# Kernel optimization log

Hardware: AMD Instinct MI355X
Metric: run time of the kernel (lower is better)

## Reference

```python
import jax, jax.numpy as jnp
import numpy as np

B, S, D, H, K = 16, 2048, 1024, 16, 31  # batch, seq, d_model, n_heads, kernel_size


def setup_inputs() -> dict:
    key = jax.random.key(0)
    ks = jax.random.split(key, 6)
    sc = 1.0 / np.sqrt(D)
    return {
        "query_sequences": jax.random.normal(ks[0], (B, S, D), jnp.float32),
        "key_sequences": jax.random.normal(ks[1], (B, S, D), jnp.float32),
        "value_sequences": jax.random.normal(ks[2], (B, S, D), jnp.float32),
        "key_value_sequence_lengths": jax.random.randint(ks[3], (B,), 1, S + 1, jnp.int32),
        "W_q": jax.random.normal(ks[4], (D, H * K), jnp.float32) * sc,  # cast_queries.weight^T
        "b_q": jnp.zeros((H * K,), jnp.float32),                        # cast_queries.bias
        "conv_bias": jnp.zeros((H,), jnp.float32),
    }


def reference(query_sequences, key_sequences, value_sequences,
              key_value_sequence_lengths, W_q, b_q, conv_bias):
    b, s, d = query_sequences.shape
    h = conv_bias.shape[0]
    k = W_q.shape[1] // h
    r = d // h
    # Generate per-position, per-head depthwise filters from the queries.
    weights = (query_sequences @ W_q + b_q).reshape(b, s, h, k)  # (B,S,H,K)
    # Split key channels into heads and reduce within each head -> (B,S,H)
    ksum = key_sequences.reshape(b, s, h, r).sum(axis=-1)
    pad_l = (k - 1) // 2
    pad_r = k - 1 - pad_l
    kpad = jnp.pad(ksum, ((0, 0), (pad_l, pad_r), (0, 0)))  # (B, S+K-1, H)
    # Cross-correlation with per-position filters:
    # out[b,t,h] = sum_j weights[b,t,h,j] * kpad[b, t+j, h]
    out = jnp.zeros((b, s, h), dtype=weights.dtype)
    for j in range(k):  # fixed small kernel loop
        out = out + weights[..., j] * kpad[:, j:j + s, :]
    out = out + conv_bias  # per-head bias
    return out.transpose(0, 2, 1)  # (B, n_heads, S)
```

## Files before the change

### kernel.cpp

```cpp
#include <hip/hip_runtime.h>
#include <hip/hip_bf16.h>

#define BB 16
#define SS 2048
#define DD 1024
#define HH 16
#define KK 31
#define HK 496

typedef float f32x16 __attribute__((ext_vector_type(16)));
typedef __bf16 bf16x8 __attribute__((ext_vector_type(8)));

__device__ __forceinline__ unsigned f2bf(float x) {
  unsigned u = __float_as_uint(x);
  unsigned r = u + 0x7FFFu + ((u >> 16) & 1u);
  return r >> 16;
}

__global__ void prep_kernel(const float* __restrict__ Wq,
                            unsigned short* __restrict__ Bimg) {
  int idx = blockIdx.x * 256 + threadIdx.x;
  int e = idx & 7;
  int lane = (idx >> 3) & 63;
  int nt = (idx >> 9) & 1;
  int w = (idx >> 10) & 7;
  int slice = (idx >> 13) & 1;
  int ks = idx >> 14;
  int k = ks * 32 + slice * 16 + (lane >> 5) * 8 + e;
  int c = w * 64 + nt * 32 + (lane & 31);
  int h = c >> 5, j = c & 31;
  float v = (j < KK) ? Wq[k * HK + h * KK + j] : 0.f;
  Bimg[idx] = (unsigned short)f2bf(v);
}

__global__ void ksum_kernel(const float* __restrict__ key,
                            float* __restrict__ ksum) {
  const int row = blockIdx.x;
  const int tid = threadIdx.x;
  const float4 v = reinterpret_cast<const float4*>(key + (size_t)row * DD)[tid];
  float p = v.x + v.y + v.z + v.w;
  p += __shfl_xor(p, 1);
  p += __shfl_xor(p, 2);
  p += __shfl_xor(p, 4);
  p += __shfl_xor(p, 8);
  if ((tid & 15) == 0) ksum[(size_t)row * HH + (tid >> 4)] = p;
}

__global__ __launch_bounds__(512, 4) void mca_kernel(
    const float* __restrict__ q, const float* __restrict__ bq,
    const float* __restrict__ convb, const float* __restrict__ ksum,
    const unsigned short* __restrict__ Bimg, float* __restrict__ out) {
  __shared__ char smem[8192];
  const int tid = threadIdx.x;
  const int w = tid >> 6, lane = tid & 63;
  const int l31 = lane & 31, hi = lane >> 5;
  const int bid = blockIdx.x;
  const int bb = bid >> 5;
  const int t0 = (bid & 31) << 6;

  char* const bA0 = smem;
  char* const bA1 = smem + 4096;

  const float* qblk = q + ((size_t)(bb * SS + t0)) * DD;
  const unsigned short* bbase = Bimg + (((size_t)w * 2) << 9) + lane * 8;

  f32x16 acc[2][2];
#pragma unroll
  for (int mt = 0; mt < 2; ++mt)
#pragma unroll
    for (int nt = 0; nt < 2; ++nt)
#pragma unroll
      for (int r = 0; r < 16; ++r) acc[mt][nt][r] = 0.f;

  const int arow = tid >> 3;
  const int ak4 = tid & 7;
  const int as = ak4 >> 2, ah = (ak4 >> 1) & 1, ae = ak4 & 1;
  const int abyte = as * 2048 + ah * 1024 + arow * 16 + ae * 8;

  auto issueA = [&](int ks, float4& rA) {
    rA = *reinterpret_cast<const float4*>(qblk + (size_t)arow * DD + ks * 32 + ak4 * 4);
  };
  auto writeA = [&](char* dst, const float4& rA) {
    unsigned u0 = f2bf(rA.x) | (f2bf(rA.y) << 16);
    unsigned u1 = f2bf(rA.z) | (f2bf(rA.w) << 16);
    *reinterpret_cast<uint2*>(dst + abyte) = make_uint2(u0, u1);
  };
  auto loadB = [&](int ks, bf16x8 pB[2][2]) {
    const unsigned short* p = bbase + (size_t)ks * 16384;
#pragma unroll
    for (int s = 0; s < 2; ++s)
#pragma unroll
      for (int nt = 0; nt < 2; ++nt)
        pB[s][nt] = *reinterpret_cast<const bf16x8*>(p + (s * 16 + nt) * 512);
  };
  auto computeT = [&](const char* bufA, const bf16x8 pB[2][2]) {
#pragma unroll
    for (int s = 0; s < 2; ++s) {
      bf16x8 a[2];
#pragma unroll
      for (int mt = 0; mt < 2; ++mt)
        a[mt] = *reinterpret_cast<const bf16x8*>(
            bufA + s * 2048 + hi * 1024 + (mt * 32 + l31) * 16);
#pragma unroll
      for (int mt = 0; mt < 2; ++mt)
#pragma unroll
        for (int nt = 0; nt < 2; ++nt)
          acc[mt][nt] = __builtin_amdgcn_mfma_f32_32x32x16_bf16(
              a[mt], pB[s][nt], acc[mt][nt], 0, 0, 0);
    }
  };
  auto barrier = [&]() {
    asm volatile("s_waitcnt lgkmcnt(0)" ::: "memory");
    __builtin_amdgcn_s_barrier();
  };

  float4 rA0, rA1;
  bf16x8 pBa[2][2], pBb[2][2];

  issueA(0, rA0);
  loadB(0, pBa);
  writeA(bA0, rA0);
  barrier();

  for (int ks2 = 0; ks2 < 15; ++ks2) {
    const int ks = ks2 * 2;
    issueA(ks + 1, rA1);
    loadB(ks + 1, pBb);
    computeT(bA0, pBa);
    writeA(bA1, rA1);
    barrier();
    issueA(ks + 2, rA0);
    loadB(ks + 2, pBa);
    computeT(bA1, pBb);
    writeA(bA0, rA0);
    barrier();
  }
  issueA(31, rA1);
  loadB(31, pBb);
  computeT(bA0, pBa);
  writeA(bA1, rA1);
  barrier();
  computeT(bA1, pBb);

  float bqv[2], cb[2];
#pragma unroll
  for (int nt = 0; nt < 2; ++nt) {
    const int h = w * 2 + nt;
    bqv[nt] = (l31 < KK) ? bq[h * KK + l31] : 0.f;
    cb[nt] = convb[h];
  }

  __syncthreads();
  float* kl = reinterpret_cast<float*>(smem);
  for (int i = tid; i < 96 * 16; i += 512) {
    int trow = i >> 4, h = i & 15;
    int t = t0 + trow - 15;
    kl[trow * 17 + h] = (t >= 0 && t < SS) ? ksum[((size_t)bb * SS + t) * HH + h] : 0.f;
  }
  __syncthreads();

#pragma unroll
  for (int mt = 0; mt < 2; ++mt)
#pragma unroll
    for (int nt = 0; nt < 2; ++nt) {
      const int h = w * 2 + nt;
#pragma unroll
      for (int r = 0; r < 16; ++r) {
        const int tl = mt * 32 + (r & 3) + 8 * (r >> 2) + 4 * hi;
        float v = (acc[mt][nt][r] + bqv[nt]) * kl[(tl + l31) * 17 + h];
        v += __shfl_xor(v, 1);
        v += __shfl_xor(v, 2);
        v += __shfl_xor(v, 4);
        v += __shfl_xor(v, 8);
        v += __shfl_xor(v, 16);
        if (l31 == r)
          out[((size_t)(bb * HH + h)) * SS + t0 + tl] = v + cb[nt];
      }
    }
}

extern "C" void kernel_launch(void* const* d_in, const int* in_sizes, int n_in,
                              void* d_out, int out_size, void* d_ws, size_t ws_size,
                              hipStream_t stream) {
  const float* q   = (const float*)d_in[0];
  const float* key = (const float*)d_in[1];
  const float* Wq  = (const float*)d_in[4];
  const float* bq  = (const float*)d_in[5];
  const float* cvb = (const float*)d_in[6];
  float* out = (float*)d_out;

  float* ksum = (float*)d_ws;
  unsigned short* Bimg = (unsigned short*)((char*)d_ws + (2 << 20));

  prep_kernel<<<2048, 256, 0, stream>>>(Wq, Bimg);
  ksum_kernel<<<BB * SS, 256, 0, stream>>>(key, ksum);
  mca_kernel<<<BB * (SS / 64), 512, 0, stream>>>(q, bq, cvb, ksum, Bimg, out);
}
```

Measured before the change: 90.31 us.

## Split heads across two blocks with 256-wide K stages and swizzled LDS

Splits the 16 heads between two blocks per 64-row tile, so each wave computes one head, and doubles the grid. The A tile is now staged 256 K-columns at a time in 32 KB double buffers with an XOR swizzle, so there are far fewer barriers. B fragments are prefetched four steps ahead in a ring of registers. Nontemporal loads and stores are added for the key reads and output writes. In exchange, each Q tile is read twice from global memory (once per head half), and each block needs 64 KB of dynamic LDS, which reduces occupancy.

```diff
diff --git a/kernel.cpp b/kernel.cpp
--- a/kernel.cpp
+++ b/kernel.cpp
@@ -9,6 +9,7 @@
 #define HK 496
 
 typedef float f32x16 __attribute__((ext_vector_type(16)));
+typedef float f32x4 __attribute__((ext_vector_type(4)));
 typedef __bf16 bf16x8 __attribute__((ext_vector_type(8)));
 
 __device__ __forceinline__ unsigned f2bf(float x) {
@@ -22,13 +23,13 @@
   int idx = blockIdx.x * 256 + threadIdx.x;
   int e = idx & 7;
   int lane = (idx >> 3) & 63;
-  int nt = (idx >> 9) & 1;
-  int w = (idx >> 10) & 7;
-  int slice = (idx >> 13) & 1;
-  int ks = idx >> 14;
-  int k = ks * 32 + slice * 16 + (lane >> 5) * 8 + e;
-  int c = w * 64 + nt * 32 + (lane & 31);
-  int h = c >> 5, j = c & 31;
+  int h8 = (idx >> 9) & 7;
+  int s = (idx >> 12) & 1;
+  int ks = (idx >> 13) & 31;
+  int nb = (idx >> 18) & 1;
+  int k = ks * 32 + s * 16 + (lane >> 5) * 8 + e;
+  int h = nb * 8 + h8;
+  int j = lane & 31;
   float v = (j < KK) ? Wq[k * HK + h * KK + j] : 0.f;
   Bimg[idx] = (unsigned short)f2bf(v);
 }
@@ -37,7 +38,8 @@
                             float* __restrict__ ksum) {
   const int row = blockIdx.x;
   const int tid = threadIdx.x;
-  const float4 v = reinterpret_cast<const float4*>(key + (size_t)row * DD)[tid];
+  const f32x4 v = __builtin_nontemporal_load(
+      reinterpret_cast<const f32x4*>(key + (size_t)row * DD) + tid);
   float p = v.x + v.y + v.z + v.w;
   p += __shfl_xor(p, 1);
   p += __shfl_xor(p, 2);
@@ -50,132 +52,138 @@
     const float* __restrict__ q, const float* __restrict__ bq,
     const float* __restrict__ convb, const float* __restrict__ ksum,
     const unsigned short* __restrict__ Bimg, float* __restrict__ out) {
-  __shared__ char smem[8192];
+  extern __shared__ char smem[];
   const int tid = threadIdx.x;
   const int w = tid >> 6, lane = tid & 63;
   const int l31 = lane & 31, hi = lane >> 5;
   const int bid = blockIdx.x;
-  const int bb = bid >> 5;
-  const int t0 = (bid & 31) << 6;
-
-  char* const bA0 = smem;
-  char* const bA1 = smem + 4096;
+  const int nb = bid & 1;
+  const int mb = bid >> 1;
+  const int bb = mb >> 5;
+  const int t0 = (mb & 31) << 6;
+
+  char* const buf0 = smem;
+  char* const buf1 = smem + 32768;
 
   const float* qblk = q + ((size_t)(bb * SS + t0)) * DD;
-  const unsigned short* bbase = Bimg + (((size_t)w * 2) << 9) + lane * 8;
-
-  f32x16 acc[2][2];
+  const unsigned short* bbase = Bimg + (size_t)nb * 262144 + w * 512 + lane * 8;
+
+  f32x16 acc[2];
 #pragma unroll
   for (int mt = 0; mt < 2; ++mt)
 #pragma unroll
-    for (int nt = 0; nt < 2; ++nt)
-#pragma unroll
-      for (int r = 0; r < 16; ++r) acc[mt][nt][r] = 0.f;
-
-  const int arow = tid >> 3;
-  const int ak4 = tid & 7;
-  const int as = ak4 >> 2, ah = (ak4 >> 1) & 1, ae = ak4 & 1;
-  const int abyte = as * 2048 + ah * 1024 + arow * 16 + ae * 8;
-
-  auto issueA = [&](int ks, float4& rA) {
-    rA = *reinterpret_cast<const float4*>(qblk + (size_t)arow * DD + ks * 32 + ak4 * 4);
-  };
-  auto writeA = [&](char* dst, const float4& rA) {
-    unsigned u0 = f2bf(rA.x) | (f2bf(rA.y) << 16);
-    unsigned u1 = f2bf(rA.z) | (f2bf(rA.w) << 16);
-    *reinterpret_cast<uint2*>(dst + abyte) = make_uint2(u0, u1);
-  };
-  auto loadB = [&](int ks, bf16x8 pB[2][2]) {
-    const unsigned short* p = bbase + (size_t)ks * 16384;
+    for (int r = 0; r < 16; ++r) acc[mt][r] = 0.f;
+
+  f32x4 rq[4];
+
+  auto issueA = [&](int p, int hf) {
+#pragma unroll
+    for (int it = 0; it < 4; ++it) {
+      const int gidx = hf * 2048 + it * 512 + tid;
+      const int row = gidx >> 6, c16 = gidx & 63;
+      rq[it] = *reinterpret_cast<const f32x4*>(qblk + (size_t)row * DD + p * 256 + c16 * 4);
+    }
+  };
+  auto writeA = [&](char* dst, int hf) {
+#pragma unroll
+    for (int it = 0; it < 4; ++it) {
+      const int gidx = hf * 2048 + it * 512 + tid;
+      const int row = gidx >> 6, c16 = gidx & 63;
+      const int ksl = c16 >> 3, sl = (c16 >> 2) & 1, h2 = (c16 >> 1) & 1, e2 = c16 & 1;
+      int byte = ksl * 4096 + sl * 2048 + h2 * 1024 + row * 16 + e2 * 8;
+      byte ^= (h2 << 4) ^ (sl << 5) ^ ((ksl & 1) << 6) ^ (((ksl >> 1) & 1) << 7) ^
+              (((ksl >> 2) & 1) << 8);
+      unsigned u0 = f2bf(rq[it].x) | (f2bf(rq[it].y) << 16);
+      unsigned u1 = f2bf(rq[it].z) | (f2bf(rq[it].w) << 16);
+      *reinterpret_cast<uint2*>(dst + byte) = make_uint2(u0, u1);
+    }
+  };
+
+  bf16x8 Bs[4][2];
+  auto loadB = [&](int ks, int slot) {
 #pragma unroll
     for (int s = 0; s < 2; ++s)
-#pragma unroll
-      for (int nt = 0; nt < 2; ++nt)
-        pB[s][nt] = *reinterpret_cast<const bf16x8*>(p + (s * 16 + nt) * 512);
-  };
-  auto computeT = [&](const char* bufA, const bf16x8 pB[2][2]) {
-#pragma unroll
-    for (int s = 0; s < 2; ++s) {
-      bf16x8 a[2];
-#pragma unroll
-      for (int mt = 0; mt < 2; ++mt)
-        a[mt] = *reinterpret_cast<const bf16x8*>(
-            bufA + s * 2048 + hi * 1024 + (mt * 32 + l31) * 16);
-#pragma unroll
-      for (int mt = 0; mt < 2; ++mt)
-#pragma unroll
-        for (int nt = 0; nt < 2; ++nt)
-          acc[mt][nt] = __builtin_amdgcn_mfma_f32_32x32x16_bf16(
-              a[mt], pB[s][nt], acc[mt][nt], 0, 0, 0);
-    }
-  };
-  auto barrier = [&]() {
+      Bs[slot][s] = *reinterpret_cast<const bf16x8*>(bbase + (size_t)ks * 8192 + s * 4096);
+  };
+  auto dsA = [&](const char* buf, int ksl, int s, int mt) -> bf16x8 {
+    int byte = ksl * 4096 + s * 2048 + hi * 1024 + (mt * 32 + l31) * 16;
+    byte ^= (hi << 4) ^ (s << 5) ^ ((ksl & 1) << 6) ^ (((ksl >> 1) & 1) << 7) ^
+            (((ksl >> 2) & 1) << 8);
+    return *reinterpret_cast<const bf16x8*>(buf + byte);
+  };
+  auto lbar = [&]() {
     asm volatile("s_waitcnt lgkmcnt(0)" ::: "memory");
     __builtin_amdgcn_s_barrier();
-  };
-
-  float4 rA0, rA1;
-  bf16x8 pBa[2][2], pBb[2][2];
-
-  issueA(0, rA0);
-  loadB(0, pBa);
-  writeA(bA0, rA0);
-  barrier();
-
-  for (int ks2 = 0; ks2 < 15; ++ks2) {
-    const int ks = ks2 * 2;
-    issueA(ks + 1, rA1);
-    loadB(ks + 1, pBb);
-    computeT(bA0, pBa);
-    writeA(bA1, rA1);
-    barrier();
-    issueA(ks + 2, rA0);
-    loadB(ks + 2, pBa);
-    computeT(bA1, pBb);
-    writeA(bA0, rA0);
-    barrier();
+    asm volatile("" ::: "memory");
+  };
+
+  loadB(0, 0);
+  loadB(1, 1);
+  loadB(2, 2);
+  loadB(3, 3);
+  issueA(0, 0);
+  writeA(buf0, 0);
+  issueA(0, 1);
+  writeA(buf0, 1);
+  lbar();
+
+#pragma unroll
+  for (int p = 0; p < 4; ++p) {
+    char* cur = (p & 1) ? buf1 : buf0;
+    char* nxt = (p & 1) ? buf0 : buf1;
+    if (p < 3) issueA(p + 1, 0);
+#pragma unroll
+    for (int st = 0; st < 8; ++st) {
+      const int ks = p * 8 + st;
+      const int slot = ks & 3;
+      bf16x8 a00 = dsA(cur, st, 0, 0);
+      bf16x8 a10 = dsA(cur, st, 0, 1);
+      acc[0] = __builtin_amdgcn_mfma_f32_32x32x16_bf16(a00, Bs[slot][0], acc[0], 0, 0, 0);
+      acc[1] = __builtin_amdgcn_mfma_f32_32x32x16_bf16(a10, Bs[slot][0], acc[1], 0, 0, 0);
+      bf16x8 a01 = dsA(cur, st, 1, 0);
+      bf16x8 a11 = dsA(cur, st, 1, 1);
+      acc[0] = __builtin_amdgcn_mfma_f32_32x32x16_bf16(a01, Bs[slot][1], acc[0], 0, 0, 0);
+      acc[1] = __builtin_amdgcn_mfma_f32_32x32x16_bf16(a11, Bs[slot][1], acc[1], 0, 0, 0);
+      if (ks + 4 < 32) loadB(ks + 4, slot);
+      if (st == 3 && p < 3) {
+        writeA(nxt, 0);
+        issueA(p + 1, 1);
+      }
+    }
+    if (p < 3) {
+      writeA(nxt, 1);
+      lbar();
+    }
   }
-  issueA(31, rA1);
-  loadB(31, pBb);
-  computeT(bA0, pBa);
-  writeA(bA1, rA1);
-  barrier();
-  computeT(bA1, pBb);
-
-  float bqv[2], cb[2];
-#pragma unroll
-  for (int nt = 0; nt < 2; ++nt) {
-    const int h = w * 2 + nt;
-    bqv[nt] = (l31 < KK) ? bq[h * KK + l31] : 0.f;
-    cb[nt] = convb[h];
-  }
+
+  const int h = nb * 8 + w;
+  const float bqv = (l31 < KK) ? bq[h * KK + l31] : 0.f;
+  const float cbv = convb[h];
 
   __syncthreads();
   float* kl = reinterpret_cast<float*>(smem);
-  for (int i = tid; i < 96 * 16; i += 512) {
-    int trow = i >> 4, h = i & 15;
+  for (int i = tid; i < 96 * 8; i += 512) {
+    int trow = i >> 3, h8 = i & 7;
     int t = t0 + trow - 15;
-    kl[trow * 17 + h] = (t >= 0 && t < SS) ? ksum[((size_t)bb * SS + t) * HH + h] : 0.f;
+    kl[trow * 9 + h8] =
+        (t >= 0 && t < SS) ? ksum[((size_t)bb * SS + t) * HH + nb * 8 + h8] : 0.f;
   }
   __syncthreads();
 
 #pragma unroll
   for (int mt = 0; mt < 2; ++mt)
 #pragma unroll
-    for (int nt = 0; nt < 2; ++nt) {
-      const int h = w * 2 + nt;
-#pragma unroll
-      for (int r = 0; r < 16; ++r) {
-        const int tl = mt * 32 + (r & 3) + 8 * (r >> 2) + 4 * hi;
-        float v = (acc[mt][nt][r] + bqv[nt]) * kl[(tl + l31) * 17 + h];
-        v += __shfl_xor(v, 1);
-        v += __shfl_xor(v, 2);
-        v += __shfl_xor(v, 4);
-        v += __shfl_xor(v, 8);
-        v += __shfl_xor(v, 16);
-        if (l31 == r)
-          out[((size_t)(bb * HH + h)) * SS + t0 + tl] = v + cb[nt];
-      }
+    for (int r = 0; r < 16; ++r) {
+      const int tl = mt * 32 + (r & 3) + 8 * (r >> 2) + 4 * hi;
+      float v = (acc[mt][r] + bqv) * kl[(tl + l31) * 9 + w];
+      v += __shfl_xor(v, 1);
+      v += __shfl_xor(v, 2);
+      v += __shfl_xor(v, 4);
+      v += __shfl_xor(v, 8);
+      v += __shfl_xor(v, 16);
+      if (l31 == r)
+        __builtin_nontemporal_store(v + cbv,
+                                    out + ((size_t)(bb * HH + h)) * SS + t0 + tl);
     }
 }
 
@@ -192,7 +200,10 @@
   float* ksum = (float*)d_ws;
   unsigned short* Bimg = (unsigned short*)((char*)d_ws + (2 << 20));
 
+  hipFuncSetAttribute((const void*)mca_kernel,
+                      hipFuncAttributeMaxDynamicSharedMemorySize, 65536);
+
   prep_kernel<<<2048, 256, 0, stream>>>(Wq, Bimg);
   ksum_kernel<<<BB * SS, 256, 0, stream>>>(key, ksum);
-  mca_kernel<<<BB * (SS / 64), 512, 0, stream>>>(q, bq, cvb, ksum, Bimg, out);
-}
+  mca_kernel<<<BB * (SS / 64) * 2, 512, 65536, stream>>>(q, bq, cvb, ksum, Bimg, out);
+}
```

New measurement: 123.1 us. 36.3% more time.

## Stage A and B tiles via direct global-to-LDS loads with double buffering

Applied to the files above, without the earlier changes.

Replaces register-staged loads of Q (fp32→bf16 converted before LDS writes) and per-thread B fragment loads with global_load_lds async copies into double-buffered LDS. Q is kept fp32 in LDS with an XOR swizzle and converted to bf16 at fragment read time, and vmcnt waits pipeline the next stage behind compute. The ksum kernel is also changed to process 16 rows per block. This raises LDS use to 80KB per block, which lowers occupancy, and adds conversion work on every fragment read.

```diff
diff --git a/kernel.cpp b/kernel.cpp
--- a/kernel.cpp
+++ b/kernel.cpp
@@ -9,12 +9,19 @@
 #define HK 496
 
 typedef float f32x16 __attribute__((ext_vector_type(16)));
+typedef float f32x4 __attribute__((ext_vector_type(4)));
 typedef __bf16 bf16x8 __attribute__((ext_vector_type(8)));
 
 __device__ __forceinline__ unsigned f2bf(float x) {
   unsigned u = __float_as_uint(x);
   unsigned r = u + 0x7FFFu + ((u >> 16) & 1u);
   return r >> 16;
+}
+
+__device__ __forceinline__ void gll16(const void* g, void* l) {
+  __builtin_amdgcn_global_load_lds(
+      (const __attribute__((address_space(1))) unsigned int*)g,
+      (__attribute__((address_space(3))) unsigned int*)l, 16, 0, 0);
 }
 
 __global__ void prep_kernel(const float* __restrict__ Wq,
@@ -33,24 +40,28 @@
   Bimg[idx] = (unsigned short)f2bf(v);
 }
 
-__global__ void ksum_kernel(const float* __restrict__ key,
-                            float* __restrict__ ksum) {
-  const int row = blockIdx.x;
+__global__ __launch_bounds__(256) void ksum_kernel(const float* __restrict__ key,
+                                                   float* __restrict__ ksum) {
   const int tid = threadIdx.x;
-  const float4 v = reinterpret_cast<const float4*>(key + (size_t)row * DD)[tid];
-  float p = v.x + v.y + v.z + v.w;
-  p += __shfl_xor(p, 1);
-  p += __shfl_xor(p, 2);
-  p += __shfl_xor(p, 4);
-  p += __shfl_xor(p, 8);
-  if ((tid & 15) == 0) ksum[(size_t)row * HH + (tid >> 4)] = p;
+  const int r0 = blockIdx.x * 16;
+#pragma unroll 4
+  for (int rr = 0; rr < 16; ++rr) {
+    const int row = r0 + rr;
+    const f32x4 v = *((const f32x4*)(key + (size_t)row * DD) + tid);
+    float p = v.x + v.y + v.z + v.w;
+    p += __shfl_xor(p, 1);
+    p += __shfl_xor(p, 2);
+    p += __shfl_xor(p, 4);
+    p += __shfl_xor(p, 8);
+    if ((tid & 15) == 0) ksum[(size_t)row * HH + (tid >> 4)] = p;
+  }
 }
 
 __global__ __launch_bounds__(512, 4) void mca_kernel(
     const float* __restrict__ q, const float* __restrict__ bq,
     const float* __restrict__ convb, const float* __restrict__ ksum,
     const unsigned short* __restrict__ Bimg, float* __restrict__ out) {
-  __shared__ char smem[8192];
+  extern __shared__ char smem[];
   const int tid = threadIdx.x;
   const int w = tid >> 6, lane = tid & 63;
   const int l31 = lane & 31, hi = lane >> 5;
@@ -58,11 +69,17 @@
   const int bb = bid >> 5;
   const int t0 = (bid & 31) << 6;
 
-  char* const bA0 = smem;
-  char* const bA1 = smem + 4096;
+  char* const A0 = smem;
+  char* const A1 = smem + 8192;
+  char* const B0 = smem + 16384;
+  char* const B1 = smem + 49152;
 
   const float* qblk = q + ((size_t)(bb * SS + t0)) * DD;
-  const unsigned short* bbase = Bimg + (((size_t)w * 2) << 9) + lane * 8;
+  const char* const BimgB = (const char*)Bimg;
+
+  const int arow = tid >> 3;
+  const int ac16 = tid & 7;
+  const float* aSrc = qblk + (size_t)arow * DD + ((ac16 ^ (arow & 7)) << 2);
 
   f32x16 acc[2][2];
 #pragma unroll
@@ -72,75 +89,71 @@
 #pragma unroll
       for (int r = 0; r < 16; ++r) acc[mt][nt][r] = 0.f;
 
-  const int arow = tid >> 3;
-  const int ak4 = tid & 7;
-  const int as = ak4 >> 2, ah = (ak4 >> 1) & 1, ae = ak4 & 1;
-  const int abyte = as * 2048 + ah * 1024 + arow * 16 + ae * 8;
-
-  auto issueA = [&](int ks, float4& rA) {
-    rA = *reinterpret_cast<const float4*>(qblk + (size_t)arow * DD + ks * 32 + ak4 * 4);
-  };
-  auto writeA = [&](char* dst, const float4& rA) {
-    unsigned u0 = f2bf(rA.x) | (f2bf(rA.y) << 16);
-    unsigned u1 = f2bf(rA.z) | (f2bf(rA.w) << 16);
-    *reinterpret_cast<uint2*>(dst + abyte) = make_uint2(u0, u1);
-  };
-  auto loadB = [&](int ks, bf16x8 pB[2][2]) {
-    const unsigned short* p = bbase + (size_t)ks * 16384;
-#pragma unroll
-    for (int s = 0; s < 2; ++s)
-#pragma unroll
-      for (int nt = 0; nt < 2; ++nt)
-        pB[s][nt] = *reinterpret_cast<const bf16x8*>(p + (s * 16 + nt) * 512);
-  };
-  auto computeT = [&](const char* bufA, const bf16x8 pB[2][2]) {
+  auto stage = [&](int ks, bool odd) {
+    char* Ad = odd ? A1 : A0;
+    char* Bd = odd ? B1 : B0;
+    gll16(aSrc + ks * 32, Ad + w * 1024);
+#pragma unroll
+    for (int r = 0; r < 4; ++r)
+      gll16(BimgB + (size_t)ks * 32768 + r * 8192 + (size_t)tid * 16,
+            Bd + r * 8192 + w * 1024);
+  };
+
+  auto afrag = [&](const char* Ad, int s, int mt) -> bf16x8 {
+    const int row = mt * 32 + l31;
+    const int u = s * 2 + hi;
+    const int g0 = (2 * u) ^ (row & 7);
+    const int g1 = (2 * u + 1) ^ (row & 7);
+    const f32x4 lo = *(const f32x4*)(Ad + row * 128 + g0 * 16);
+    const f32x4 hh = *(const f32x4*)(Ad + row * 128 + g1 * 16);
+    unsigned p0, p1, p2, p3;
+    asm("v_cvt_pk_bf16_f32 %0, %1, %2" : "=v"(p0) : "v"(lo.x), "v"(lo.y));
+    asm("v_cvt_pk_bf16_f32 %0, %1, %2" : "=v"(p1) : "v"(lo.z), "v"(lo.w));
+    asm("v_cvt_pk_bf16_f32 %0, %1, %2" : "=v"(p2) : "v"(hh.x), "v"(hh.y));
+    asm("v_cvt_pk_bf16_f32 %0, %1, %2" : "=v"(p3) : "v"(hh.z), "v"(hh.w));
+    union { unsigned u4[4]; bf16x8 b; } cv;
+    cv.u4[0] = p0; cv.u4[1] = p1; cv.u4[2] = p2; cv.u4[3] = p3;
+    return cv.b;
+  };
+  auto bfrag = [&](const char* Bd, int s, int nt) -> bf16x8 {
+    return *(const bf16x8*)(Bd + s * 16384 + nt * 1024 + w * 2048 + lane * 16);
+  };
+  auto compute = [&](const char* Ad, const char* Bd) {
 #pragma unroll
     for (int s = 0; s < 2; ++s) {
-      bf16x8 a[2];
-#pragma unroll
-      for (int mt = 0; mt < 2; ++mt)
-        a[mt] = *reinterpret_cast<const bf16x8*>(
-            bufA + s * 2048 + hi * 1024 + (mt * 32 + l31) * 16);
-#pragma unroll
-      for (int mt = 0; mt < 2; ++mt)
-#pragma unroll
-        for (int nt = 0; nt < 2; ++nt)
-          acc[mt][nt] = __builtin_amdgcn_mfma_f32_32x32x16_bf16(
-              a[mt], pB[s][nt], acc[mt][nt], 0, 0, 0);
+      bf16x8 b0 = bfrag(Bd, s, 0);
+      bf16x8 b1 = bfrag(Bd, s, 1);
+      bf16x8 a0 = afrag(Ad, s, 0);
+      bf16x8 a1 = afrag(Ad, s, 1);
+      acc[0][0] = __builtin_amdgcn_mfma_f32_32x32x16_bf16(a0, b0, acc[0][0], 0, 0, 0);
+      acc[1][0] = __builtin_amdgcn_mfma_f32_32x32x16_bf16(a1, b0, acc[1][0], 0, 0, 0);
+      acc[0][1] = __builtin_amdgcn_mfma_f32_32x32x16_bf16(a0, b1, acc[0][1], 0, 0, 0);
+      acc[1][1] = __builtin_amdgcn_mfma_f32_32x32x16_bf16(a1, b1, acc[1][1], 0, 0, 0);
     }
   };
-  auto barrier = [&]() {
-    asm volatile("s_waitcnt lgkmcnt(0)" ::: "memory");
+
+  stage(0, false);
+  stage(1, true);
+  asm volatile("s_waitcnt vmcnt(5)" ::: "memory");
+  __builtin_amdgcn_sched_barrier(0);
+  __builtin_amdgcn_s_barrier();
+
+#pragma unroll 2
+  for (int ks = 0; ks < 30; ++ks) {
+    const bool odd = ks & 1;
+    compute(odd ? A1 : A0, odd ? B1 : B0);
     __builtin_amdgcn_s_barrier();
-  };
-
-  float4 rA0, rA1;
-  bf16x8 pBa[2][2], pBb[2][2];
-
-  issueA(0, rA0);
-  loadB(0, pBa);
-  writeA(bA0, rA0);
-  barrier();
-
-  for (int ks2 = 0; ks2 < 15; ++ks2) {
-    const int ks = ks2 * 2;
-    issueA(ks + 1, rA1);
-    loadB(ks + 1, pBb);
-    computeT(bA0, pBa);
-    writeA(bA1, rA1);
-    barrier();
-    issueA(ks + 2, rA0);
-    loadB(ks + 2, pBa);
-    computeT(bA1, pBb);
-    writeA(bA0, rA0);
-    barrier();
-  }
-  issueA(31, rA1);
-  loadB(31, pBb);
-  computeT(bA0, pBa);
-  writeA(bA1, rA1);
-  barrier();
-  computeT(bA1, pBb);
+    __builtin_amdgcn_sched_barrier(0);
+    stage(ks + 2, odd);
+    asm volatile("s_waitcnt vmcnt(5)" ::: "memory");
+    __builtin_amdgcn_sched_barrier(0);
+    __builtin_amdgcn_s_barrier();
+  }
+  compute(A0, B0);
+  asm volatile("s_waitcnt vmcnt(0)" ::: "memory");
+  __builtin_amdgcn_sched_barrier(0);
+  __builtin_amdgcn_s_barrier();
+  compute(A1, B1);
 
   float bqv[2], cb[2];
 #pragma unroll
@@ -192,7 +205,10 @@
   float* ksum = (float*)d_ws;
   unsigned short* Bimg = (unsigned short*)((char*)d_ws + (2 << 20));
 
+  hipFuncSetAttribute((const void*)mca_kernel,
+                      hipFuncAttributeMaxDynamicSharedMemorySize, 81920);
+
   prep_kernel<<<2048, 256, 0, stream>>>(Wq, Bimg);
-  ksum_kernel<<<BB * SS, 256, 0, stream>>>(key, ksum);
-  mca_kernel<<<BB * (SS / 64), 512, 0, stream>>>(q, bq, cvb, ksum, Bimg, out);
-}
+  ksum_kernel<<<2048, 256, 0, stream>>>(key, ksum);
+  mca_kernel<<<BB * (SS / 64), 512, 81920, stream>>>(q, bq, cvb, ksum, Bimg, out);
+}
```

After: 97.13 us. 1.08x slower.
